# Kernel optimization log

Measured on AMD Instinct MI355X. Metric: run time of the kernel, lower is better.

The kernel has to match this reference:

```python
import jax, jax.numpy as jnp
import numpy as np


def _conv_bn_relu(x, w, b, stride):
    # Conv2d(k=3, pad=1) with eval-mode BatchNorm folded into (w, b) at setup, then ReLU.
    y = jax.lax.conv_general_dilated(x, w, (stride, stride), ((1, 1), (1, 1)),
                                     dimension_numbers=('NCHW', 'OIHW', 'NCHW'))
    return jax.nn.relu(y + b[None, :, None, None])


def _affine_grid(theta, H, W):
    # torch.nn.functional.affine_grid, align_corners=False
    xs = (2.0 * jnp.arange(W, dtype=theta.dtype) + 1.0) / W - 1.0  # [W]
    ys = (2.0 * jnp.arange(H, dtype=theta.dtype) + 1.0) / H - 1.0  # [H]
    gx = theta[:, 0, 0, None, None] * xs[None, None, :] + theta[:, 0, 1, None, None] * ys[None, :, None] + theta[:, 0, 2, None, None]
    gy = theta[:, 1, 0, None, None] * xs[None, None, :] + theta[:, 1, 1, None, None] * ys[None, :, None] + theta[:, 1, 2, None, None]
    return jnp.stack([gx, gy], axis=-1)  # [B,H,W,2]


def _grid_sample_bilinear_zeros(im, grid):
    # torch.nn.functional.grid_sample, mode='bilinear', padding_mode='zeros', align_corners=False
    B, C, H, W = im.shape
    ix = ((grid[..., 0] + 1.0) * W - 1.0) * 0.5  # [B,H,W] pixel x coords
    iy = ((grid[..., 1] + 1.0) * H - 1.0) * 0.5
    x0 = jnp.floor(ix); y0 = jnp.floor(iy)
    x1 = x0 + 1.0;      y1 = y0 + 1.0
    wx1 = ix - x0; wx0 = 1.0 - wx1
    wy1 = iy - y0; wy0 = 1.0 - wy1
    imt = jnp.transpose(im, (0, 2, 3, 1))  # BHWC for channel-last gather
    bidx = jnp.arange(B)[:, None, None]

    def gather(xf, yf):
        valid = ((xf >= 0) & (xf <= W - 1) & (yf >= 0) & (yf <= H - 1)).astype(im.dtype)
        xi = jnp.clip(xf.astype(jnp.int32), 0, W - 1)
        yi = jnp.clip(yf.astype(jnp.int32), 0, H - 1)
        return imt[bidx, yi, xi] * valid[..., None]  # [B,H,W,C]

    out = (gather(x0, y0) * (wx0 * wy0)[..., None]
           + gather(x1, y0) * (wx1 * wy0)[..., None]
           + gather(x0, y1) * (wx0 * wy1)[..., None]
           + gather(x1, y1) * (wx1 * wy1)[..., None])
    return jnp.transpose(out, (0, 3, 1, 2))  # back to NCHW


def _forward(im_tensor, w1, b1, w2, b2, w3, b3, w4, b4, w5, b5, w6, b6,
             fw1, fb1, fw2, fb2, fw3, fb3):
    B, _, H, W = im_tensor.shape
    x1 = _conv_bn_relu(im_tensor, w1, b1, 1)
    x2 = _conv_bn_relu(jnp.concatenate([x1, im_tensor], 1), w2, b2, 2)
    x3 = _conv_bn_relu(x2, w3, b3, 1)
    x4 = _conv_bn_relu(jnp.concatenate([x3, x2], 1), w4, b4, 2)
    x5 = _conv_bn_relu(x4, w5, b5, 1)
    xs = _conv_bn_relu(jnp.concatenate([x5, x4], 1), w6, b6, 2)
    xs = xs.reshape(B, -1)  # [B, 24*(H/8)*(W/8)]
    h = jax.nn.relu(xs @ fw1.T + fb1)
    h = jax.nn.relu(h @ fw2.T + fb2)
    sz = h @ fw3.T + fb3  # [B, 4]
    # mode == 'normal': vectorized theta construction (original loops over batch)
    theta = jnp.zeros((B, 2, 3), dtype=im_tensor.dtype)
    theta = theta.at[:, 0, 0].set(jax.nn.sigmoid(sz[:, 0]))
    theta = theta.at[:, 0, 2].set(jnp.tanh(sz[:, 2]))
    theta = theta.at[:, 1, 1].set(jax.nn.sigmoid(sz[:, 1]))
    theta = theta.at[:, 1, 2].set(jnp.tanh(sz[:, 3]))
    grid = _affine_grid(theta, H, W)
    im_cropped = _grid_sample_bilinear_zeros(im_tensor, grid)
    return im_cropped, theta


def setup_inputs() -> dict:
    key = jax.random.key(0)
    B, H, W = 32, 256, 256
    keys = iter(jax.random.split(key, 64))
    nk = lambda: next(keys)
    im = jax.random.normal(nk(), (B, 1, H, W), jnp.float32)

    def conv_params(cin, cout):
        w = jax.random.normal(nk(), (cout, cin, 3, 3), jnp.float32) * (1.0 / np.sqrt(cin * 9))
        b = jax.random.normal(nk(), (cout,), jnp.float32) * 0.01
        # eval-mode BatchNorm params, folded into conv weight/bias (exact same math)
        gamma = 1.0 + 0.1 * jax.random.normal(nk(), (cout,), jnp.float32)
        beta = 0.1 * jax.random.normal(nk(), (cout,), jnp.float32)
        mean = 0.1 * jax.random.normal(nk(), (cout,), jnp.float32)
        var = jnp.abs(1.0 + 0.1 * jax.random.normal(nk(), (cout,), jnp.float32))
        scale = gamma / jnp.sqrt(var + 1e-5)
        return w * scale[:, None, None, None], b * scale + (beta - mean * scale)

    w1, b1 = conv_params(1, 8)
    w2, b2 = conv_params(9, 8)
    w3, b3 = conv_params(8, 16)
    w4, b4 = conv_params(24, 16)
    w5, b5 = conv_params(16, 24)
    w6, b6 = conv_params(40, 24)
    feat = 24 * (H // 8) * (W // 8)
    fw1 = jax.random.normal(nk(), (1024, feat), jnp.float32) * (1.0 / np.sqrt(feat))
    fb1 = jnp.zeros((1024,), jnp.float32)
    fw2 = jax.random.normal(nk(), (32, 1024), jnp.float32) * (1.0 / np.sqrt(1024))
    fb2 = jnp.zeros((32,), jnp.float32)
    fw3 = jax.random.normal(nk(), (4, 32), jnp.float32) * 0.01  # small perturbation of zero-init
    fb3 = jnp.array([1.0, 1.0, 0.0, 0.0], jnp.float32)
    return dict(im_tensor=im, w1=w1, b1=b1, w2=w2, b2=b2, w3=w3, b3=b3,
                w4=w4, b4=b4, w5=w5, b5=b5, w6=w6, b6=b6,
                fw1=fw1, fb1=fb1, fw2=fw2, fb2=fb2, fw3=fw3, fb3=fb3)


def reference(im_tensor, w1, b1, w2, b2, w3, b3, w4, b4, w5, b5, w6, b6,
              fw1, fb1, fw2, fb2, fw3, fb3):
    return _forward(im_tensor, w1, b1, w2, b2, w3, b3, w4, b4, w5, b5, w6, b6,
                    fw1, fb1, fw2, fb2, fw3, fb3)
```

## Files before the change

### kernel.cpp

```cpp
#include <hip/hip_runtime.h>
#include <hip/hip_bf16.h>

template <int CIN1, int CIN2, int COUT, int CG, int CCH, int MINW>
__global__ __launch_bounds__(256, MINW) void convq_k(
    const float* __restrict__ in1, const float* __restrict__ in2,
    const float* __restrict__ w,
    const float* __restrict__ bias,
    float* __restrict__ out,
    int Hin, int Win)
{
    constexpr int CIN = CIN1 + CIN2;
    constexpr int NG  = COUT / CG;
    constexpr int NCH = CIN / CCH;
    constexpr int P   = 34;
    constexpr int NF4 = 10;
    constexpr int WL  = NF4 * 4;
    constexpr int E4  = CCH * P * NF4;
    constexpr int NLD = (E4 + 255) / 256;
    __shared__ __align__(16) float Xs[2][CCH][P][WL];

    const int Ho = Hin, Wo = Win;
    const int tpr = Wo / 32, tpc = Ho / 32;
    int bid = blockIdx.x;
    const int tx = bid % tpr; bid /= tpr;
    const int ty = bid % tpc; bid /= tpc;
    const int g  = bid % NG;  bid /= NG;
    const int b  = bid;
    const int cbase = g * CG;

    const int tid = threadIdx.x;
    const int lx = tid & 15, ly = tid >> 4;

    const int y0 = ty * 32 - 1;
    const int xA = tx * 32 - 4;
    const int HW = Hin * Win;

    float acc[CG][4];
#pragma unroll
    for (int co = 0; co < CG; ++co) {
        float bv = bias[cbase + co];
#pragma unroll
        for (int p = 0; p < 4; ++p) acc[co][p] = bv;
    }

    int cA[NLD], lOff[NLD], em[NLD];
    bool eok[NLD], rowk[NLD], f4[NLD];
    const float* b1p[NLD];
    const float* b2p[NLD];
#pragma unroll
    for (int l = 0; l < NLD; ++l) {
        int e = tid + l * 256;
        eok[l] = (e < E4);
        int ee = eok[l] ? e : 0;
        int c  = ee / (P * NF4), r = ee % (P * NF4);
        int py = r / NF4,        jx = r % NF4;
        cA[l]   = c;
        lOff[l] = ee;
        int gy = y0 + py, c0 = xA + jx * 4;
        rowk[l] = eok[l] && ((unsigned)gy < (unsigned)Hin);
        f4[l]   = (c0 >= 0) && (c0 + 4 <= Win);
        em[l] = 0;
#pragma unroll
        for (int e2 = 0; e2 < 4; ++e2)
            if ((unsigned)(c0 + e2) < (unsigned)Win) em[l] |= 1 << e2;
        b1p[l] = (const float*)((const char*)in1 +
                 ((ptrdiff_t)(b * CIN1 + c) * HW + (ptrdiff_t)gy * Win + c0)
                 * (ptrdiff_t)sizeof(float));
        b2p[l] = (CIN2 > 0)
            ? (const float*)((const char*)in2 +
                 ((ptrdiff_t)(b * CIN2 + c - CIN1) * HW + (ptrdiff_t)gy * Win + c0)
                 * (ptrdiff_t)sizeof(float))
            : b1p[l];
    }

    float4 stg[NLD];

    auto issue = [&](int cc) {
        const size_t adv = (size_t)cc * HW;
#pragma unroll
        for (int l = 0; l < NLD; ++l) {
            float4 v = {0.0f, 0.0f, 0.0f, 0.0f};
            if (rowk[l]) {
                int ci = cc + cA[l];
                const float* p = (CIN2 == 0 || ci < CIN1) ? (b1p[l] + adv)
                                                          : (b2p[l] + adv);
                if (f4[l]) {
                    v = *(const float4*)p;
                } else {
                    float* vp = reinterpret_cast<float*>(&v);
#pragma unroll
                    for (int e2 = 0; e2 < 4; ++e2)
                        if (em[l] & (1 << e2)) vp[e2] = p[e2];
                }
            }
            stg[l] = v;
        }
    };
    auto commit = [&](int bf) {
        float4* dst = (float4*)&Xs[0][0][0][0] + (size_t)bf * (CCH * P * NF4);
#pragma unroll
        for (int l = 0; l < NLD; ++l)
            if (eok[l]) dst[lOff[l]] = stg[l];
    };

    issue(0);
    commit(0);
    __syncthreads();

    const int cb = 2 * lx + 3;

    int buf = 0;
    for (int ch = 0; ch < NCH; ++ch) {
        if (ch + 1 < NCH) issue((ch + 1) * CCH);
#pragma unroll
        for (int c = 0; c < CCH; ++c) {
#pragma unroll
            for (int ky = 0; ky < 3; ++ky) {
                const float* x0 = &Xs[buf][c][2 * ly + ky][cb];
                const float* x1 = &Xs[buf][c][2 * ly + ky + 1][cb];
                float a0 = x0[0], a1 = x0[1], a2 = x0[2], a3 = x0[3];
                float b0 = x1[0], b1v = x1[1], b2v = x1[2], b3 = x1[3];
#pragma unroll
                for (int co = 0; co < CG; ++co) {
                    const float* wp = w +
                        ((size_t)(cbase + co) * CIN + ch * CCH + c) * 9 + ky * 3;
                    float w0 = wp[0], w1 = wp[1], w2 = wp[2];
                    acc[co][0] = fmaf(a0, w0, acc[co][0]);
                    acc[co][0] = fmaf(a1, w1, acc[co][0]);
                    acc[co][0] = fmaf(a2, w2, acc[co][0]);
                    acc[co][1] = fmaf(a1, w0, acc[co][1]);
                    acc[co][1] = fmaf(a2, w1, acc[co][1]);
                    acc[co][1] = fmaf(a3, w2, acc[co][1]);
                    acc[co][2] = fmaf(b0, w0, acc[co][2]);
                    acc[co][2] = fmaf(b1v, w1, acc[co][2]);
                    acc[co][2] = fmaf(b2v, w2, acc[co][2]);
                    acc[co][3] = fmaf(b1v, w0, acc[co][3]);
                    acc[co][3] = fmaf(b2v, w1, acc[co][3]);
                    acc[co][3] = fmaf(b3, w2, acc[co][3]);
                }
            }
        }
        if (ch + 1 < NCH) {
            commit(buf ^ 1);
            __syncthreads();
            buf ^= 1;
        }
    }

    const int oy = ty * 32 + 2 * ly;
    const int ox = tx * 32 + 2 * lx;
#pragma unroll
    for (int co = 0; co < CG; ++co)
#pragma unroll
        for (int dy = 0; dy < 2; ++dy) {
            float2 v;
            v.x = fmaxf(acc[co][dy * 2 + 0], 0.0f);
            v.y = fmaxf(acc[co][dy * 2 + 1], 0.0f);
            *(float2*)&out[((size_t)(b * COUT + cbase + co) * Ho + oy + dy) * Wo + ox] = v;
        }
}

template <int CIN1, int CIN2, int COUT, int CG, int MINW>
__global__ __launch_bounds__(256, MINW) void convq2_k(
    const float* __restrict__ in1, const float* __restrict__ in2,
    const float* __restrict__ w,
    const float* __restrict__ bias,
    float* __restrict__ out,
    int Hin, int Win)
{
    constexpr int CIN = CIN1 + CIN2;
    constexpr int NG  = COUT / CG;
    constexpr int P   = 66;
    constexpr int NF4 = 18;
    constexpr int WL  = NF4 * 4;
    constexpr int E4  = P * NF4;
    constexpr int NLD = (E4 + 255) / 256;
    __shared__ __align__(16) float Xs[2][P][WL];

    const int Ho = Hin / 2, Wo = Win / 2;
    const int tpr = Wo / 32, tpc = Ho / 32;
    int bid = blockIdx.x;
    const int tx = bid % tpr; bid /= tpr;
    const int ty = bid % tpc; bid /= tpc;
    const int g  = bid % NG;  bid /= NG;
    const int b  = bid;
    const int cbase = g * CG;

    const int tid = threadIdx.x;
    const int lx = tid & 15, ly = tid >> 4;

    const int y0 = ty * 64 - 1;
    const int xA = tx * 64 - 4;
    const int HW = Hin * Win;

    float acc[CG][4];
#pragma unroll
    for (int co = 0; co < CG; ++co) {
        float bv = bias[cbase + co];
#pragma unroll
        for (int p = 0; p < 4; ++p) acc[co][p] = bv;
    }

    int lOff[NLD], em[NLD];
    bool eok[NLD], rowk[NLD], f4[NLD];
    const float* b1p[NLD];
    const float* b2p[NLD];
#pragma unroll
    for (int l = 0; l < NLD; ++l) {
        int e = tid + l * 256;
        eok[l] = (e < E4);
        int ee = eok[l] ? e : 0;
        int py = ee / NF4, jx = ee % NF4;
        lOff[l] = ee;
        int gy = y0 + py, c0 = xA + jx * 4;
        rowk[l] = eok[l] && ((unsigned)gy < (unsigned)Hin);
        f4[l]   = (c0 >= 0) && (c0 + 4 <= Win);
        em[l] = 0;
#pragma unroll
        for (int e2 = 0; e2 < 4; ++e2)
            if ((unsigned)(c0 + e2) < (unsigned)Win) em[l] |= 1 << e2;
        b1p[l] = (const float*)((const char*)in1 +
                 ((ptrdiff_t)(b * CIN1) * HW + (ptrdiff_t)gy * Win + c0)
                 * (ptrdiff_t)sizeof(float));
        b2p[l] = (CIN2 > 0)
            ? (const float*)((const char*)in2 +
                 ((ptrdiff_t)(b * CIN2 - CIN1) * HW + (ptrdiff_t)gy * Win + c0)
                 * (ptrdiff_t)sizeof(float))
            : b1p[l];
    }

    float4 stg[NLD];

    auto issue = [&](int ci) {
        const size_t adv = (size_t)ci * HW;
#pragma unroll
        for (int l = 0; l < NLD; ++l) {
            float4 v = {0.0f, 0.0f, 0.0f, 0.0f};
            if (rowk[l]) {
                const float* p = (CIN2 == 0 || ci < CIN1) ? (b1p[l] + adv)
                                                          : (b2p[l] + adv);
                if (f4[l]) {
                    v = *(const float4*)p;
                } else {
                    float* vp = reinterpret_cast<float*>(&v);
#pragma unroll
                    for (int e2 = 0; e2 < 4; ++e2)
                        if (em[l] & (1 << e2)) vp[e2] = p[e2];
                }
            }
            stg[l] = v;
        }
    };
    auto commit = [&](int bf) {
        float4* dst = (float4*)&Xs[0][0][0] + (size_t)bf * E4;
#pragma unroll
        for (int l = 0; l < NLD; ++l)
            if (eok[l]) dst[lOff[l]] = stg[l];
    };

    issue(0);
    commit(0);
    __syncthreads();

    const int cb = 4 * lx + 3;

    int buf = 0;
    for (int ch = 0; ch < CIN; ++ch) {
        if (ch + 1 < CIN) issue(ch + 1);
#pragma unroll
        for (int ky = 0; ky < 3; ++ky) {
            const float* x0 = &Xs[buf][4 * ly + ky][cb];
            const float* x1 = &Xs[buf][4 * ly + ky + 2][cb];
            float v0 = x0[0], v1 = x0[1], v2 = x0[2], v3 = x0[3], v4 = x0[4];
            float u0 = x1[0], u1 = x1[1], u2 = x1[2], u3 = x1[3], u4 = x1[4];
#pragma unroll
            for (int co = 0; co < CG; ++co) {
                const float* wp = w + ((size_t)(cbase + co) * CIN + ch) * 9 + ky * 3;
                float w0 = wp[0], w1 = wp[1], w2 = wp[2];
                acc[co][0] = fmaf(v0, w0, acc[co][0]);
                acc[co][0] = fmaf(v1, w1, acc[co][0]);
                acc[co][0] = fmaf(v2, w2, acc[co][0]);
                acc[co][1] = fmaf(v2, w0, acc[co][1]);
                acc[co][1] = fmaf(v3, w1, acc[co][1]);
                acc[co][1] = fmaf(v4, w2, acc[co][1]);
                acc[co][2] = fmaf(u0, w0, acc[co][2]);
                acc[co][2] = fmaf(u1, w1, acc[co][2]);
                acc[co][2] = fmaf(u2, w2, acc[co][2]);
                acc[co][3] = fmaf(u2, w0, acc[co][3]);
                acc[co][3] = fmaf(u3, w1, acc[co][3]);
                acc[co][3] = fmaf(u4, w2, acc[co][3]);
            }
        }
        if (ch + 1 < CIN) {
            commit(buf ^ 1);
            __syncthreads();
            buf ^= 1;
        }
    }

    const int oy = ty * 32 + 2 * ly;
    const int ox = tx * 32 + 2 * lx;
#pragma unroll
    for (int co = 0; co < CG; ++co)
#pragma unroll
        for (int dy = 0; dy < 2; ++dy) {
            float2 v;
            v.x = fmaxf(acc[co][dy * 2 + 0], 0.0f);
            v.y = fmaxf(acc[co][dy * 2 + 1], 0.0f);
            *(float2*)&out[((size_t)(b * COUT + cbase + co) * Ho + oy + dy) * Wo + ox] = v;
        }
}

template <int CIN1, int CIN2, int COUT, int CG, int STRIDE, int CCH, int MINW>
__global__ __launch_bounds__(256, MINW) void conv2p_k(
    const float* __restrict__ in1, const float* __restrict__ in2,
    const float* __restrict__ w,
    const float* __restrict__ bias,
    float* __restrict__ out,
    int Hin, int Win)
{
    constexpr int CIN = CIN1 + CIN2;
    constexpr int NG  = COUT / CG;
    constexpr int NCH = CIN / CCH;
    constexpr int P   = 16 * STRIDE + 2;
    constexpr int NF4 = (STRIDE == 1) ? 10 : 17;
    constexpr int WL  = NF4 * 4;
    constexpr int E4  = CCH * P * NF4;
    constexpr int NLD = (E4 + 255) / 256;
    __shared__ __align__(16) float Xs[2][CCH][P][WL];

    const int Ho = Hin / STRIDE, Wo = Win / STRIDE;
    const int tpr = Wo / 32, tpc = Ho / 16;
    int bid = blockIdx.x;
    const int tx = bid % tpr; bid /= tpr;
    const int ty = bid % tpc; bid /= tpc;
    const int g  = bid % NG;  bid /= NG;
    const int b  = bid;
    const int cbase = g * CG;

    const int tid = threadIdx.x;
    const int lx = tid & 15, ly = tid >> 4;

    const int y0 = ty * 16 * STRIDE - 1;
    const int xA = tx * 32 * STRIDE - 4;
    const int HW = Hin * Win;

    float2 acc[CG];
#pragma unroll
    for (int co = 0; co < CG; ++co) {
        float bv = bias[cbase + co];
        acc[co].x = bv; acc[co].y = bv;
    }

    int cA[NLD], lOff[NLD], em[NLD];
    bool eok[NLD], rowk[NLD], f4[NLD];
    const float* b1p[NLD];
    const float* b2p[NLD];
#pragma unroll
    for (int l = 0; l < NLD; ++l) {
        int e = tid + l * 256;
        eok[l] = (e < E4);
        int ee = eok[l] ? e : 0;
        int c  = ee / (P * NF4), r = ee % (P * NF4);
        int py = r / NF4,        jx = r % NF4;
        cA[l]   = c;
        lOff[l] = ee;
        int gy = y0 + py, c0 = xA + jx * 4;
        rowk[l] = eok[l] && ((unsigned)gy < (unsigned)Hin);
        f4[l]   = (c0 >= 0) && (c0 + 4 <= Win);
        em[l] = 0;
#pragma unroll
        for (int e2 = 0; e2 < 4; ++e2)
            if ((unsigned)(c0 + e2) < (unsigned)Win) em[l] |= 1 << e2;
        b1p[l] = (const float*)((const char*)in1 +
                 ((ptrdiff_t)(b * CIN1 + c) * HW + (ptrdiff_t)gy * Win + c0)
                 * (ptrdiff_t)sizeof(float));
        b2p[l] = (CIN2 > 0)
            ? (const float*)((const char*)in2 +
                 ((ptrdiff_t)(b * CIN2 + c - CIN1) * HW + (ptrdiff_t)gy * Win + c0)
                 * (ptrdiff_t)sizeof(float))
            : b1p[l];
    }

    float4 stg[NLD];

    auto issue = [&](int cc) {
        const size_t adv = (size_t)cc * HW;
#pragma unroll
        for (int l = 0; l < NLD; ++l) {
            float4 v = {0.0f, 0.0f, 0.0f, 0.0f};
            if (rowk[l]) {
                int ci = cc + cA[l];
                const float* p = (CIN2 == 0 || ci < CIN1) ? (b1p[l] + adv)
                                                          : (b2p[l] + adv);
                if (f4[l]) {
                    v = *(const float4*)p;
                } else {
                    float* vp = reinterpret_cast<float*>(&v);
#pragma unroll
                    for (int e2 = 0; e2 < 4; ++e2)
                        if (em[l] & (1 << e2)) vp[e2] = p[e2];
                }
            }
            stg[l] = v;
        }
    };
    auto commit = [&](int bf) {
        float4* dst = (float4*)&Xs[0][0][0][0] + (size_t)bf * (CCH * P * NF4);
#pragma unroll
        for (int l = 0; l < NLD; ++l)
            if (eok[l]) dst[lOff[l]] = stg[l];
    };

    issue(0);
    commit(0);
    __syncthreads();

    const int cb = (2 * lx) * STRIDE + 3;

    int buf = 0;
    for (int ch = 0; ch < NCH; ++ch) {
        if (ch + 1 < NCH) issue((ch + 1) * CCH);
#pragma unroll
        for (int c = 0; c < CCH; ++c) {
#pragma unroll
            for (int ky = 0; ky < 3; ++ky) {
                const float* xr = &Xs[buf][c][ly * STRIDE + ky][0];
                float2 r0, r1, r2;
                r0.x = xr[cb + 0]; r0.y = xr[cb + 0 + STRIDE];
                r1.x = xr[cb + 1]; r1.y = xr[cb + 1 + STRIDE];
                r2.x = xr[cb + 2]; r2.y = xr[cb + 2 + STRIDE];
#pragma unroll
                for (int co = 0; co < CG; ++co) {
                    const float* wp = w +
                        ((size_t)(cbase + co) * CIN + ch * CCH + c) * 9 + ky * 3;
                    float w0 = wp[0], w1 = wp[1], w2 = wp[2];
                    float2 a = acc[co];
                    a.x = fmaf(r0.x, w0, a.x); a.y = fmaf(r0.y, w0, a.y);
                    a.x = fmaf(r1.x, w1, a.x); a.y = fmaf(r1.y, w1, a.y);
                    a.x = fmaf(r2.x, w2, a.x); a.y = fmaf(r2.y, w2, a.y);
                    acc[co] = a;
                }
            }
        }
        if (ch + 1 < NCH) {
            commit(buf ^ 1);
            __syncthreads();
            buf ^= 1;
        }
    }

    const int oy = ty * 16 + ly;
    const int ox = tx * 32 + 2 * lx;
#pragma unroll
    for (int co = 0; co < CG; ++co) {
        float2 v;
        v.x = fmaxf(acc[co].x, 0.0f);
        v.y = fmaxf(acc[co].y, 0.0f);
        *(float2*)&out[((size_t)(b * COUT + cbase + co) * Ho + oy) * Wo + ox] = v;
    }
}

#define FC1_K 24576
#define FC1_N 1024
#define FC1_M 32
#define FC1_KS 32
#define FC1_KC 768
#define FC1_KP 64
#define FC1_NT 64

__global__ __launch_bounds__(256) void fc1_stage_k(
    const float* __restrict__ xs,
    const float* __restrict__ fw1,
    float* __restrict__ part)
{
    __shared__ __align__(16) float As[FC1_KP][36];
    __shared__ __align__(16) float Bs[FC1_KP][66];

    const int tid = threadIdx.x;
    const int n0 = blockIdx.x * FC1_NT;
    const int ks = blockIdx.y;
    const int k0 = ks * FC1_KC;
    const int lane = tid & 63;
    const int grp = tid >> 6;

    const int m4 = (tid & 7) * 4;
    const int n2 = (tid >> 3) * 2;

    float acc[4][2];
#pragma unroll
    for (int i = 0; i < 4; ++i)
#pragma unroll
        for (int j = 0; j < 2; ++j) acc[i][j] = 0.0f;

    for (int p = 0; p < FC1_KC / FC1_KP; ++p) {
        const int kc = k0 + p * FC1_KP;
#pragma unroll
        for (int r = 0; r < 8; ++r) {
            int m = grp * 8 + r;
            As[lane][m] = xs[(size_t)m * FC1_K + kc + lane];
        }
#pragma unroll
        for (int r = 0; r < 16; ++r) {
            int nl = grp * 16 + r;
            Bs[lane][nl] = fw1[(size_t)(n0 + nl) * FC1_K + kc + lane];
        }
        __syncthreads();
#pragma unroll 8
        for (int k = 0; k < FC1_KP; ++k) {
            float4 a = *(const float4*)&As[k][m4];
            float2 bv = *(const float2*)&Bs[k][n2];
            acc[0][0] += a.x * bv.x; acc[0][1] += a.x * bv.y;
            acc[1][0] += a.y * bv.x; acc[1][1] += a.y * bv.y;
            acc[2][0] += a.z * bv.x; acc[2][1] += a.z * bv.y;
            acc[3][0] += a.w * bv.x; acc[3][1] += a.w * bv.y;
        }
        __syncthreads();
    }
#pragma unroll
    for (int i = 0; i < 4; ++i)
#pragma unroll
        for (int j = 0; j < 2; ++j)
            part[((size_t)ks * FC1_M + (m4 + i)) * FC1_N + n0 + n2 + j] = acc[i][j];
}

__global__ __launch_bounds__(256) void fc1_reduce_k(
    const float* __restrict__ part, const float* __restrict__ fb1,
    float* __restrict__ h1)
{
    int idx = blockIdx.x * 256 + threadIdx.x;
    int n = idx & (FC1_N - 1);
    int m = idx >> 10;
    float s = fb1[n];
#pragma unroll
    for (int ks = 0; ks < FC1_KS; ++ks)
        s += part[((size_t)ks * FC1_M + m) * FC1_N + n];
    h1[idx] = fmaxf(s, 0.0f);
}

__global__ __launch_bounds__(256) void fc2_k(
    const float* __restrict__ h1, const float* __restrict__ fw2,
    const float* __restrict__ fb2, float* __restrict__ h2)
{
    __shared__ float hs[1024];
    const int m = blockIdx.x;
    const int tid = threadIdx.x;
    for (int i = tid; i < 1024; i += 256) hs[i] = h1[m * 1024 + i];
    __syncthreads();
    const int wave = tid >> 6, lane = tid & 63;
#pragma unroll 1
    for (int nn = 0; nn < 8; ++nn) {
        int n = wave * 8 + nn;
        float p = 0.0f;
        for (int k = lane; k < 1024; k += 64)
            p += fw2[n * 1024 + k] * hs[k];
#pragma unroll
        for (int off = 32; off; off >>= 1) p += __shfl_xor(p, off);
        if (lane == 0) h2[m * 32 + n] = fmaxf(p + fb2[n], 0.0f);
    }
}

__global__ void fc3_theta_k(
    const float* __restrict__ h2, const float* __restrict__ fw3,
    const float* __restrict__ fb3, float* __restrict__ theta_out)
{
    int t = threadIdx.x;
    if (t >= 128) return;
    int m = t >> 2, j = t & 3;
    float s = fb3[j];
#pragma unroll
    for (int k = 0; k < 32; ++k) s += h2[m * 32 + k] * fw3[j * 32 + k];
    float* th = theta_out + m * 6;
    if (j == 0)      { th[0] = 1.0f / (1.0f + expf(-s)); th[1] = 0.0f; }
    else if (j == 1) { th[4] = 1.0f / (1.0f + expf(-s)); th[3] = 0.0f; }
    else if (j == 2) { th[2] = tanhf(s); }
    else             { th[5] = tanhf(s); }
}

__global__ __launch_bounds__(256) void sampler_k(
    const float* __restrict__ im, const float* __restrict__ theta,
    float* __restrict__ out)
{
    int idx = blockIdx.x * 256 + threadIdx.x;
    int x = idx & 255;
    int y = (idx >> 8) & 255;
    int b = idx >> 16;
    const float* th = theta + b * 6;
    float xsn = (2.0f * x + 1.0f) * (1.0f / 256.0f) - 1.0f;
    float ysn = (2.0f * y + 1.0f) * (1.0f / 256.0f) - 1.0f;
    float gx = th[0] * xsn + th[1] * ysn + th[2];
    float gy = th[3] * xsn + th[4] * ysn + th[5];
    float ix = ((gx + 1.0f) * 256.0f - 1.0f) * 0.5f;
    float iy = ((gy + 1.0f) * 256.0f - 1.0f) * 0.5f;
    float x0 = floorf(ix), y0 = floorf(iy);
    float wx1 = ix - x0, wy1 = iy - y0;
    float wx0 = 1.0f - wx1, wy0 = 1.0f - wy1;
    const float* src = im + (size_t)b * 65536;

    auto g = [&](float xf, float yf) -> float {
        if (xf < 0.0f || xf > 255.0f || yf < 0.0f || yf > 255.0f) return 0.0f;
        int xi = (int)xf, yi = (int)yf;
        return src[yi * 256 + xi];
    };
    float v00 = g(x0, y0);
    float v10 = g(x0 + 1.0f, y0);
    float v01 = g(x0, y0 + 1.0f);
    float v11 = g(x0 + 1.0f, y0 + 1.0f);
    out[idx] = v00 * wx0 * wy0 + v10 * wx1 * wy0 + v01 * wx0 * wy1 + v11 * wx1 * wy1;
}

extern "C" void kernel_launch(void* const* d_in, const int* in_sizes, int n_in,
                              void* d_out, int out_size, void* d_ws, size_t ws_size,
                              hipStream_t stream)
{
    const float* im  = (const float*)d_in[0];
    const float* w1  = (const float*)d_in[1];  const float* b1 = (const float*)d_in[2];
    const float* w2  = (const float*)d_in[3];  const float* b2 = (const float*)d_in[4];
    const float* w3  = (const float*)d_in[5];  const float* b3 = (const float*)d_in[6];
    const float* w4  = (const float*)d_in[7];  const float* b4 = (const float*)d_in[8];
    const float* w5  = (const float*)d_in[9];  const float* b5 = (const float*)d_in[10];
    const float* w6  = (const float*)d_in[11]; const float* b6 = (const float*)d_in[12];
    const float* fw1 = (const float*)d_in[13]; const float* fb1 = (const float*)d_in[14];
    const float* fw2 = (const float*)d_in[15]; const float* fb2 = (const float*)d_in[16];
    const float* fw3 = (const float*)d_in[17]; const float* fb3 = (const float*)d_in[18];

    float* out = (float*)d_out;
    float* ws  = (float*)d_ws;

    float* x2   = ws + 0;
    float* x1c  = ws + 4194304;
    float* x3   = ws + 4194304;
    float* x4   = ws + 12582912;
    float* x5   = ws + 4194304;
    float* x6   = ws + 14680064;
    float* part = ws + 0;
    float* h1   = ws + 1048576;
    float* h2   = ws + 1081344;

    float* theta = out + 32 * 65536;

    for (int c = 0; c < 2; ++c) {
        const float* imc = im + (size_t)c * 16 * 65536;
        convq_k<1, 0, 8, 8, 1, 4><<<16 * 1 * 8 * 8, 256, 0, stream>>>(
            imc, nullptr, w1, b1, x1c, 256, 256);
        conv2p_k<8, 1, 8, 8, 2, 1, 6><<<16 * 8 * 4, 256, 0, stream>>>(
            x1c, imc, w2, b2, x2 + (size_t)c * 2097152, 256, 256);
    }
    convq_k<8, 0, 16, 8, 2, 4><<<32 * 2 * 4 * 4, 256, 0, stream>>>(
        x2, nullptr, w3, b3, x3, 128, 128);
    convq2_k<16, 8, 16, 4, 4><<<32 * 4 * 2 * 2, 256, 0, stream>>>(
        x3, x2, w4, b4, x4, 128, 128);
    convq_k<16, 0, 24, 6, 2, 4><<<32 * 4 * 2 * 2, 256, 0, stream>>>(
        x4, nullptr, w5, b5, x5, 64, 64);
    convq2_k<24, 16, 24, 3, 4><<<32 * 8 * 1 * 1, 256, 0, stream>>>(
        x5, x4, w6, b6, x6, 64, 64);

    fc1_stage_k<<<dim3(16, FC1_KS), 256, 0, stream>>>(x6, fw1, part);
    fc1_reduce_k<<<128, 256, 0, stream>>>(part, fb1, h1);
    fc2_k<<<32, 256, 0, stream>>>(h1, fw2, fb2, h2);
    fc3_theta_k<<<1, 128, 0, stream>>>(h2, fw3, fb3, theta);

    sampler_k<<<8192, 256, 0, stream>>>(im, theta, out);
}
```

Before: 307.6 us.

## Fuse FC tail kernels, vectorize fc1 weight loads, retune conv kernel choice and batching

Merges fc1 reduction, fc2 and fc3/theta into one per-sample kernel, removing two launches and the h1/h2 round trips through global memory. Switches fc1 weight staging to float4 loads transposed into shared memory. Adds a large-workspace path that runs the first two convs over the whole batch instead of two halves, and swaps kernel variants for conv2 (convq2_k) and conv6 (conv2p_k). These selections change tiling and occupancy, and the fused tail puts fc2 behind a serialized per-sample reduction.

```diff
diff --git a/kernel.cpp b/kernel.cpp
--- a/kernel.cpp
+++ b/kernel.cpp
@@ -487,6 +487,9 @@
     const int m4 = (tid & 7) * 4;
     const int n2 = (tid >> 3) * 2;
 
+    const int bk4 = (tid & 15) * 4;
+    const int bnl = tid >> 4;
+
     float acc[4][2];
 #pragma unroll
     for (int i = 0; i < 4; ++i)
@@ -501,9 +504,13 @@
             As[lane][m] = xs[(size_t)m * FC1_K + kc + lane];
         }
 #pragma unroll
-        for (int r = 0; r < 16; ++r) {
-            int nl = grp * 16 + r;
-            Bs[lane][nl] = fw1[(size_t)(n0 + nl) * FC1_K + kc + lane];
+        for (int r = 0; r < 4; ++r) {
+            int nl = r * 16 + bnl;
+            float4 v = *(const float4*)&fw1[(size_t)(n0 + nl) * FC1_K + kc + bk4];
+            Bs[bk4 + 0][nl] = v.x;
+            Bs[bk4 + 1][nl] = v.y;
+            Bs[bk4 + 2][nl] = v.z;
+            Bs[bk4 + 3][nl] = v.w;
         }
         __syncthreads();
 #pragma unroll 8
@@ -524,29 +531,26 @@
             part[((size_t)ks * FC1_M + (m4 + i)) * FC1_N + n0 + n2 + j] = acc[i][j];
 }
 
-__global__ __launch_bounds__(256) void fc1_reduce_k(
+__global__ __launch_bounds__(256) void fc_tail_k(
     const float* __restrict__ part, const float* __restrict__ fb1,
-    float* __restrict__ h1)
-{
-    int idx = blockIdx.x * 256 + threadIdx.x;
-    int n = idx & (FC1_N - 1);
-    int m = idx >> 10;
-    float s = fb1[n];
-#pragma unroll
-    for (int ks = 0; ks < FC1_KS; ++ks)
-        s += part[((size_t)ks * FC1_M + m) * FC1_N + n];
-    h1[idx] = fmaxf(s, 0.0f);
-}
-
-__global__ __launch_bounds__(256) void fc2_k(
-    const float* __restrict__ h1, const float* __restrict__ fw2,
-    const float* __restrict__ fb2, float* __restrict__ h2)
+    const float* __restrict__ fw2,  const float* __restrict__ fb2,
+    const float* __restrict__ fw3,  const float* __restrict__ fb3,
+    float* __restrict__ theta_out)
 {
     __shared__ float hs[1024];
+    __shared__ float h2s[32];
     const int m = blockIdx.x;
     const int tid = threadIdx.x;
-    for (int i = tid; i < 1024; i += 256) hs[i] = h1[m * 1024 + i];
+
+    for (int n = tid; n < FC1_N; n += 256) {
+        float s = fb1[n];
+#pragma unroll
+        for (int ks = 0; ks < FC1_KS; ++ks)
+            s += part[((size_t)ks * FC1_M + m) * FC1_N + n];
+        hs[n] = fmaxf(s, 0.0f);
+    }
     __syncthreads();
+
     const int wave = tid >> 6, lane = tid & 63;
 #pragma unroll 1
     for (int nn = 0; nn < 8; ++nn) {
@@ -556,25 +560,21 @@
             p += fw2[n * 1024 + k] * hs[k];
 #pragma unroll
         for (int off = 32; off; off >>= 1) p += __shfl_xor(p, off);
-        if (lane == 0) h2[m * 32 + n] = fmaxf(p + fb2[n], 0.0f);
-    }
-}
-
-__global__ void fc3_theta_k(
-    const float* __restrict__ h2, const float* __restrict__ fw3,
-    const float* __restrict__ fb3, float* __restrict__ theta_out)
-{
-    int t = threadIdx.x;
-    if (t >= 128) return;
-    int m = t >> 2, j = t & 3;
-    float s = fb3[j];
-#pragma unroll
-    for (int k = 0; k < 32; ++k) s += h2[m * 32 + k] * fw3[j * 32 + k];
-    float* th = theta_out + m * 6;
-    if (j == 0)      { th[0] = 1.0f / (1.0f + expf(-s)); th[1] = 0.0f; }
-    else if (j == 1) { th[4] = 1.0f / (1.0f + expf(-s)); th[3] = 0.0f; }
-    else if (j == 2) { th[2] = tanhf(s); }
-    else             { th[5] = tanhf(s); }
+        if (lane == 0) h2s[n] = fmaxf(p + fb2[n], 0.0f);
+    }
+    __syncthreads();
+
+    if (tid < 4) {
+        int j = tid;
+        float s = fb3[j];
+#pragma unroll
+        for (int k = 0; k < 32; ++k) s += h2s[k] * fw3[j * 32 + k];
+        float* th = theta_out + m * 6;
+        if (j == 0)      { th[0] = 1.0f / (1.0f + expf(-s)); th[1] = 0.0f; }
+        else if (j == 1) { th[4] = 1.0f / (1.0f + expf(-s)); th[3] = 0.0f; }
+        else if (j == 2) { th[2] = tanhf(s); }
+        else             { th[5] = tanhf(s); }
+    }
 }
 
 __global__ __launch_bounds__(256) void sampler_k(
@@ -627,38 +627,61 @@
     float* out = (float*)d_out;
     float* ws  = (float*)d_ws;
 
+    float* theta = out + 32 * 65536;
+
+    const bool big = ws_size >= (size_t)20971520 * 4;
+
     float* x2   = ws + 0;
-    float* x1c  = ws + 4194304;
-    float* x3   = ws + 4194304;
-    float* x4   = ws + 12582912;
-    float* x5   = ws + 4194304;
-    float* x6   = ws + 14680064;
     float* part = ws + 0;
-    float* h1   = ws + 1048576;
-    float* h2   = ws + 1081344;
-
-    float* theta = out + 32 * 65536;
-
-    for (int c = 0; c < 2; ++c) {
-        const float* imc = im + (size_t)c * 16 * 65536;
-        convq_k<1, 0, 8, 8, 1, 4><<<16 * 1 * 8 * 8, 256, 0, stream>>>(
-            imc, nullptr, w1, b1, x1c, 256, 256);
-        conv2p_k<8, 1, 8, 8, 2, 1, 6><<<16 * 8 * 4, 256, 0, stream>>>(
-            x1c, imc, w2, b2, x2 + (size_t)c * 2097152, 256, 256);
-    }
-    convq_k<8, 0, 16, 8, 2, 4><<<32 * 2 * 4 * 4, 256, 0, stream>>>(
-        x2, nullptr, w3, b3, x3, 128, 128);
-    convq2_k<16, 8, 16, 4, 4><<<32 * 4 * 2 * 2, 256, 0, stream>>>(
-        x3, x2, w4, b4, x4, 128, 128);
-    convq_k<16, 0, 24, 6, 2, 4><<<32 * 4 * 2 * 2, 256, 0, stream>>>(
-        x4, nullptr, w5, b5, x5, 64, 64);
-    convq2_k<24, 16, 24, 3, 4><<<32 * 8 * 1 * 1, 256, 0, stream>>>(
-        x5, x4, w6, b6, x6, 64, 64);
-
-    fc1_stage_k<<<dim3(16, FC1_KS), 256, 0, stream>>>(x6, fw1, part);
-    fc1_reduce_k<<<128, 256, 0, stream>>>(part, fb1, h1);
-    fc2_k<<<32, 256, 0, stream>>>(h1, fw2, fb2, h2);
-    fc3_theta_k<<<1, 128, 0, stream>>>(h2, fw3, fb3, theta);
+
+    if (big) {
+        float* x1 = ws + 4194304;
+        float* x3 = ws + 4194304;
+        float* x4 = ws + 12582912;
+        float* x5 = ws + 14680064;
+        float* x6 = ws + 17825792;
+
+        convq_k<1, 0, 8, 8, 1, 4><<<2048, 256, 0, stream>>>(
+            im, nullptr, w1, b1, x1, 256, 256);
+        convq2_k<8, 1, 8, 8, 4><<<512, 256, 0, stream>>>(
+            x1, im, w2, b2, x2, 256, 256);
+        convq_k<8, 0, 16, 8, 2, 4><<<1024, 256, 0, stream>>>(
+            x2, nullptr, w3, b3, x3, 128, 128);
+        convq2_k<16, 8, 16, 4, 4><<<512, 256, 0, stream>>>(
+            x3, x2, w4, b4, x4, 128, 128);
+        convq_k<16, 0, 24, 6, 2, 4><<<512, 256, 0, stream>>>(
+            x4, nullptr, w5, b5, x5, 64, 64);
+        conv2p_k<24, 16, 24, 4, 2, 1, 6><<<384, 256, 0, stream>>>(
+            x5, x4, w6, b6, x6, 64, 64);
+
+        fc1_stage_k<<<dim3(16, FC1_KS), 256, 0, stream>>>(x6, fw1, part);
+        fc_tail_k<<<32, 256, 0, stream>>>(part, fb1, fw2, fb2, fw3, fb3, theta);
+    } else {
+        float* x1c = ws + 4194304;
+        float* x3  = ws + 4194304;
+        float* x4  = ws + 12582912;
+        float* x5  = ws + 4194304;
+        float* x6  = ws + 14680064;
+
+        for (int c = 0; c < 2; ++c) {
+            const float* imc = im + (size_t)c * 16 * 65536;
+            convq_k<1, 0, 8, 8, 1, 4><<<1024, 256, 0, stream>>>(
+                imc, nullptr, w1, b1, x1c, 256, 256);
+            convq2_k<8, 1, 8, 8, 4><<<256, 256, 0, stream>>>(
+                x1c, imc, w2, b2, x2 + (size_t)c * 2097152, 256, 256);
+        }
+        convq_k<8, 0, 16, 8, 2, 4><<<1024, 256, 0, stream>>>(
+            x2, nullptr, w3, b3, x3, 128, 128);
+        convq2_k<16, 8, 16, 4, 4><<<512, 256, 0, stream>>>(
+            x3, x2, w4, b4, x4, 128, 128);
+        convq_k<16, 0, 24, 6, 2, 4><<<512, 256, 0, stream>>>(
+            x4, nullptr, w5, b5, x5, 64, 64);
+        conv2p_k<24, 16, 24, 4, 2, 1, 6><<<384, 256, 0, stream>>>(
+            x5, x4, w6, b6, x6, 64, 64);
+
+        fc1_stage_k<<<dim3(16, FC1_KS), 256, 0, stream>>>(x6, fw1, part);
+        fc_tail_k<<<32, 256, 0, stream>>>(part, fb1, fw2, fb2, fw3, fb3, theta);
+    }
 
     sampler_k<<<8192, 256, 0, stream>>>(im, theta, out);
 }
```

Measured after the change: 283.3 us. 1.09x faster.
